# Kernel tuning notes

Hardware: AMD Instinct MI355X
Metric: run time of the kernel (lower is better)

Reference implementation:

```python
import jax, jax.numpy as jnp
import numpy as np

N_NODES = 50000
N_EDGES = 1_600_000
D_IN = 512
D_OUT = 512


def setup_inputs() -> dict:
    key = jax.random.key(0)
    k_x, k_w, k_b, k_r, k_c, k_e = jax.random.split(key, 6)
    x = jax.random.normal(k_x, (N_NODES, D_IN), dtype=jnp.float32)
    stdv = 1.0 / np.sqrt(D_OUT)
    weight = jax.random.uniform(k_w, (D_IN, D_OUT), minval=-stdv, maxval=stdv, dtype=jnp.float32)
    bias = jax.random.uniform(k_b, (D_OUT,), minval=-stdv, maxval=stdv, dtype=jnp.float32)
    row = jax.random.randint(k_r, (N_EDGES,), 0, N_NODES, dtype=jnp.int32)
    col = jax.random.randint(k_c, (N_EDGES,), 0, N_NODES, dtype=jnp.int32)
    edge_weight = jax.random.uniform(k_e, (N_EDGES,), dtype=jnp.float32)
    return {"x": x, "weight": weight, "bias": bias, "row": row, "col": col, "edge_weight": edge_weight}


def reference(x, weight, bias, row, col, edge_weight):
    # support = X @ W   [N, D_OUT]
    support = x @ weight
    # spmm: out[i] = sum_{e: row[e]==i} edge_weight[e] * support[col[e]]
    msgs = edge_weight[:, None] * support[col]  # [E, D_OUT]
    out = jax.ops.segment_sum(msgs, row, num_segments=N_NODES)
    return out + bias
```

## Files before the change

### kernel.cpp

```cpp
#include <hip/hip_runtime.h>
#include <hip/hip_fp16.h>

#define D_DIM 512
#define BM 128
#define BN 128
#define BK 64

typedef _Float16 h8 __attribute__((ext_vector_type(8)));
typedef _Float16 h4 __attribute__((ext_vector_type(4)));
typedef float f32x4 __attribute__((ext_vector_type(4)));

#define LDS_PTR(p) ((__attribute__((address_space(3))) void*)(p))
#define GLB_PTR(p) ((const __attribute__((address_space(1))) void*)(p))


__global__ void k_zero(int* __restrict__ counts, int n) {
    int i = blockIdx.x * blockDim.x + threadIdx.x;
    if (i < n) counts[i] = 0;
}

__global__ void k_count(const int* __restrict__ row, int* __restrict__ counts, int E) {
    int e = blockIdx.x * blockDim.x + threadIdx.x;
    if (e < E) atomicAdd(&counts[row[e]], 1);
}

__global__ void k_scan_part(const int* __restrict__ counts, int* __restrict__ offsets,
                            int* __restrict__ bsum, int n) {
    __shared__ int s[1024];
    int t = threadIdx.x;
    int i = blockIdx.x * 1024 + t;
    int v = (i < n) ? counts[i] : 0;
    s[t] = v;
    __syncthreads();
    for (int off = 1; off < 1024; off <<= 1) {
        int x = (t >= off) ? s[t - off] : 0;
        __syncthreads();
        s[t] += x;
        __syncthreads();
    }
    if (i < n) offsets[i] = s[t] - v;
    if (t == 1023) bsum[blockIdx.x] = s[t];
}

__global__ void k_scan_top(int* __restrict__ bsum, int* __restrict__ offsets, int nb, int n) {
    int t = threadIdx.x;
    int v = (t < nb) ? bsum[t] : 0;
    int orig = v;
    for (int off = 1; off < 64; off <<= 1) {
        int u = __shfl_up(v, off, 64);
        if (t >= off) v += u;
    }
    if (t < nb) bsum[t] = v - orig;
    if (t == nb - 1) offsets[n] = v;
}

__global__ void k_scan_add(int* __restrict__ offsets, int* __restrict__ cursor,
                           const int* __restrict__ bsum, int n) {
    int i = blockIdx.x * 1024 + threadIdx.x;
    if (i < n) {
        int o = offsets[i] + bsum[blockIdx.x];
        offsets[i] = o;
        cursor[i] = o;
    }
}

__global__ void k_scatter(const int* __restrict__ row, const int* __restrict__ col,
                          const float* __restrict__ ew, int* __restrict__ cursor,
                          uint2* __restrict__ packed, int E) {
    int e = blockIdx.x * blockDim.x + threadIdx.x;
    if (e < E) {
        int r = row[e];
        int pos = atomicAdd(&cursor[r], 1);
        packed[pos] = make_uint2((unsigned)col[e], __float_as_uint(ew[e]));
    }
}


__global__ void k_wt(const float* __restrict__ w, _Float16* __restrict__ wt) {
    __shared__ _Float16 tile[32][33];
    int bx = blockIdx.x & 15, by = blockIdx.x >> 4;
    int tx = threadIdx.x & 31, ty = threadIdx.x >> 5;
    for (int r = 0; r < 32; r += 8)
        tile[ty + r][tx] = (_Float16)w[(size_t)(by * 32 + ty + r) * 512 + bx * 32 + tx];
    __syncthreads();
    for (int r = 0; r < 32; r += 8)
        wt[(size_t)(bx * 32 + ty + r) * 512 + by * 32 + tx] = tile[tx][ty + r];
}


__launch_bounds__(256)
__global__ void k_gemm(const float* __restrict__ x, const _Float16* __restrict__ wt,
                       _Float16* __restrict__ sup, int M) {
    __shared__ __align__(16) unsigned char As[BM * BK * 2];
    __shared__ __align__(16) unsigned char Bs[BN * BK * 2];

    const int t = threadIdx.x;
    const int lane = t & 63, w = t >> 6;
    const int wr = w >> 1, wc = w & 1;
    const int m0 = blockIdx.x * BM, n0 = blockIdx.y * BN;

    f32x4 acc[4][4] = {};

    const int ar_t = t >> 4;
    const int ac_t = (t & 15) * 4;
    const int bn_t = t >> 3;
    const int bk_sw = ((t & 7) * 16) ^ (((t >> 3) & 7) << 4);

    for (int kt = 0; kt < D_DIM / BK; ++kt) {
        const int k0 = kt * BK;
        for (int j = 0; j < 4; ++j) {
            int n = j * 32 + bn_t;
            const char* src = (const char*)(wt + (size_t)(n0 + n) * 512 + k0) + bk_sw;
            __builtin_amdgcn_global_load_lds(GLB_PTR(src), LDS_PTR(Bs + j * 4096 + t * 16),
                                             16, 0, 0);
        }
        for (int i = 0; i < 8; ++i) {
            int r = i * 16 + ar_t;
            int g = m0 + r;
            if (g >= M) g = M - 1;
            const float4 v = *(const float4*)(x + (size_t)g * 512 + k0 + ac_t);
            h4 hv;
            hv[0] = (_Float16)v.x; hv[1] = (_Float16)v.y;
            hv[2] = (_Float16)v.z; hv[3] = (_Float16)v.w;
            int addr = r * 128 + ((ac_t * 2) ^ ((r & 7) << 4));
            *(h4*)(As + addr) = hv;
        }
        __syncthreads();

        for (int ks = 0; ks < 2; ++ks) {
            h8 af[4], bf[4];
            const int kb = ks * 64 + ((lane >> 4) * 8) * 2;
#pragma unroll
            for (int mb = 0; mb < 4; ++mb) {
                int r = wr * 64 + mb * 16 + (lane & 15);
                af[mb] = *(const h8*)(As + r * 128 + (kb ^ ((r & 7) << 4)));
            }
#pragma unroll
            for (int nb = 0; nb < 4; ++nb) {
                int n = wc * 64 + nb * 16 + (lane & 15);
                bf[nb] = *(const h8*)(Bs + n * 128 + (kb ^ ((n & 7) << 4)));
            }
#pragma unroll
            for (int mb = 0; mb < 4; ++mb)
#pragma unroll
                for (int nb = 0; nb < 4; ++nb)
                    acc[mb][nb] = __builtin_amdgcn_mfma_f32_16x16x32_f16(
                        af[mb], bf[nb], acc[mb][nb], 0, 0, 0);
        }
        __syncthreads();
    }

    const int cr = (lane >> 4) * 4, cc = lane & 15;
#pragma unroll
    for (int mb = 0; mb < 4; ++mb) {
#pragma unroll
        for (int nb = 0; nb < 4; ++nb) {
            int gn = n0 + wc * 64 + nb * 16 + cc;
#pragma unroll
            for (int q = 0; q < 4; ++q) {
                int gm = m0 + wr * 64 + mb * 16 + cr + q;
                if (gm < M)
                    sup[(size_t)gm * 512 + gn] = (_Float16)acc[mb][nb][q];
            }
        }
    }
}


__global__ void k_spmm(const _Float16* __restrict__ sup, const uint2* __restrict__ packed,
                       const int* __restrict__ offsets, const float* __restrict__ bias,
                       float* __restrict__ out, int M) {
    const int i = blockIdx.x * 4 + (threadIdx.x >> 6);
    if (i >= M) return;
    const int l = threadIdx.x & 63;
    const int s0 = offsets[i], s1 = offsets[i + 1];
    const _Float16* __restrict__ supl = sup + l * 8;

    float acc[8];
    {
        const float4 b0 = *(const float4*)(bias + l * 8);
        const float4 b1 = *(const float4*)(bias + l * 8 + 4);
        acc[0] = b0.x; acc[1] = b0.y; acc[2] = b0.z; acc[3] = b0.w;
        acc[4] = b1.x; acc[5] = b1.y; acc[6] = b1.z; acc[7] = b1.w;
    }

    int e = s0;
    if ((e & 1) && e < s1) {
        uint2 p = packed[e];
        float wgt = __uint_as_float(p.y);
        h8 h = *(const h8*)(supl + (size_t)p.x * 512);
#pragma unroll
        for (int j = 0; j < 8; ++j) acc[j] += wgt * (float)h[j];
        ++e;
    }
    for (; e + 8 <= s1; e += 8) {
        const uint4 q0 = *(const uint4*)(packed + e);
        const uint4 q1 = *(const uint4*)(packed + e + 2);
        const uint4 q2 = *(const uint4*)(packed + e + 4);
        const uint4 q3 = *(const uint4*)(packed + e + 6);
        const h8 h0 = *(const h8*)(supl + (size_t)q0.x * 512);
        const h8 h1 = *(const h8*)(supl + (size_t)q0.z * 512);
        const h8 h2 = *(const h8*)(supl + (size_t)q1.x * 512);
        const h8 h3 = *(const h8*)(supl + (size_t)q1.z * 512);
        const h8 h4v = *(const h8*)(supl + (size_t)q2.x * 512);
        const h8 h5 = *(const h8*)(supl + (size_t)q2.z * 512);
        const h8 h6 = *(const h8*)(supl + (size_t)q3.x * 512);
        const h8 h7 = *(const h8*)(supl + (size_t)q3.z * 512);
        const float w0 = __uint_as_float(q0.y), w1 = __uint_as_float(q0.w);
        const float w2 = __uint_as_float(q1.y), w3 = __uint_as_float(q1.w);
        const float w4 = __uint_as_float(q2.y), w5 = __uint_as_float(q2.w);
        const float w6 = __uint_as_float(q3.y), w7 = __uint_as_float(q3.w);
#pragma unroll
        for (int j = 0; j < 8; ++j) {
            float a = acc[j];
            a += w0 * (float)h0[j];
            a += w1 * (float)h1[j];
            a += w2 * (float)h2[j];
            a += w3 * (float)h3[j];
            a += w4 * (float)h4v[j];
            a += w5 * (float)h5[j];
            a += w6 * (float)h6[j];
            a += w7 * (float)h7[j];
            acc[j] = a;
        }
    }
    for (; e < s1; ++e) {
        uint2 p = packed[e];
        float wgt = __uint_as_float(p.y);
        h8 h = *(const h8*)(supl + (size_t)p.x * 512);
#pragma unroll
        for (int j = 0; j < 8; ++j) acc[j] += wgt * (float)h[j];
    }

    float4 o0 = {acc[0], acc[1], acc[2], acc[3]};
    float4 o1 = {acc[4], acc[5], acc[6], acc[7]};
    *(float4*)(out + (size_t)i * 512 + l * 8) = o0;
    *(float4*)(out + (size_t)i * 512 + l * 8 + 4) = o1;
}


extern "C" void kernel_launch(void* const* d_in, const int* in_sizes, int n_in,
                              void* d_out, int out_size, void* d_ws, size_t ws_size,
                              hipStream_t stream) {
    const float* x      = (const float*)d_in[0];
    const float* weight = (const float*)d_in[1];
    const float* bias   = (const float*)d_in[2];
    const int*   row    = (const int*)d_in[3];
    const int*   col    = (const int*)d_in[4];
    const float* ew     = (const float*)d_in[5];
    const int M = in_sizes[0] / D_DIM;
    const int E = in_sizes[3];
    float* out = (float*)d_out;

    char* ws = (char*)d_ws;
    size_t off = 0;
    auto alloc = [&](size_t bytes) {
        void* p = ws + off;
        off = (off + bytes + 255) & ~(size_t)255;
        return p;
    };
    _Float16* sup  = (_Float16*)alloc((size_t)M * D_DIM * 2);
    _Float16* wt   = (_Float16*)alloc((size_t)512 * 512 * 2);
    int* counts    = (int*)alloc((size_t)M * 4);
    int* offsets   = (int*)alloc((size_t)(M + 1) * 4);
    int* cursor    = (int*)alloc((size_t)M * 4);
    int* bsum      = (int*)alloc(64 * 4);
    uint2* packed  = (uint2*)alloc((size_t)E * 8);
    (void)ws_size; (void)n_in; (void)out_size;

    k_zero<<<(M + 255) / 256, 256, 0, stream>>>(counts, M);
    k_count<<<(E + 255) / 256, 256, 0, stream>>>(row, counts, E);
    const int SB = (M + 1023) / 1024;
    k_scan_part<<<SB, 1024, 0, stream>>>(counts, offsets, bsum, M);
    k_scan_top<<<1, 64, 0, stream>>>(bsum, offsets, SB, M);
    k_scan_add<<<SB, 1024, 0, stream>>>(offsets, cursor, bsum, M);
    k_scatter<<<(E + 255) / 256, 256, 0, stream>>>(row, col, ew, cursor, packed, E);

    k_wt<<<256, 256, 0, stream>>>(weight, wt);
    dim3 gg((M + BM - 1) / BM, D_DIM / BN);
    k_gemm<<<gg, 256, 0, stream>>>(x, wt, sup, M);

    k_spmm<<<(M + 3) / 4, 256, 0, stream>>>(sup, packed, offsets, bias, out, M);
}
```

Measured before the change: 649.1 us.

## Widen GEMM tile to 128x256, remap blocks per XCD, use nontemporal SpMM I/O

The GEMM tile grows from 128x128 to 128x256, so each block covers half the output width. Each wave now computes 128x64 with 32 accumulators, which halves how often the x tile is re-read and converted. Block IDs are remapped so that neighbouring M tiles land on the same XCD, improving L2 locality. The SpMM uses nontemporal loads for the packed edge stream and nontemporal stores for the output, and the zero kernel becomes hipMemsetAsync. The larger tile raises register and LDS pressure and halves the number of GEMM blocks.

```diff
diff --git a/kernel.cpp b/kernel.cpp
--- a/kernel.cpp
+++ b/kernel.cpp
@@ -3,21 +3,17 @@
 
 #define D_DIM 512
 #define BM 128
-#define BN 128
+#define BN 256
 #define BK 64
 
 typedef _Float16 h8 __attribute__((ext_vector_type(8)));
 typedef _Float16 h4 __attribute__((ext_vector_type(4)));
 typedef float f32x4 __attribute__((ext_vector_type(4)));
+typedef unsigned int u32x4 __attribute__((ext_vector_type(4)));
 
 #define LDS_PTR(p) ((__attribute__((address_space(3))) void*)(p))
 #define GLB_PTR(p) ((const __attribute__((address_space(1))) void*)(p))
 
-
-__global__ void k_zero(int* __restrict__ counts, int n) {
-    int i = blockIdx.x * blockDim.x + threadIdx.x;
-    if (i < n) counts[i] = 0;
-}
 
 __global__ void k_count(const int* __restrict__ row, int* __restrict__ counts, int E) {
     int e = blockIdx.x * blockDim.x + threadIdx.x;
@@ -90,16 +86,20 @@
 
 __launch_bounds__(256)
 __global__ void k_gemm(const float* __restrict__ x, const _Float16* __restrict__ wt,
-                       _Float16* __restrict__ sup, int M) {
+                       _Float16* __restrict__ sup, int M, int nwg) {
     __shared__ __align__(16) unsigned char As[BM * BK * 2];
     __shared__ __align__(16) unsigned char Bs[BN * BK * 2];
 
+    const int orig = blockIdx.x;
+    const int q = nwg >> 3, r = nwg & 7;
+    const int xcd = orig & 7, idx = orig >> 3;
+    const int wgid = (xcd < r ? xcd * (q + 1) : r * (q + 1) + (xcd - r) * q) + idx;
+    const int m0 = (wgid >> 1) * BM, n0 = (wgid & 1) * BN;
+
     const int t = threadIdx.x;
     const int lane = t & 63, w = t >> 6;
-    const int wr = w >> 1, wc = w & 1;
-    const int m0 = blockIdx.x * BM, n0 = blockIdx.y * BN;
-
-    f32x4 acc[4][4] = {};
+
+    f32x4 acc[8][4] = {};
 
     const int ar_t = t >> 4;
     const int ac_t = (t & 15) * 4;
@@ -108,40 +108,40 @@
 
     for (int kt = 0; kt < D_DIM / BK; ++kt) {
         const int k0 = kt * BK;
-        for (int j = 0; j < 4; ++j) {
+        for (int j = 0; j < 8; ++j) {
             int n = j * 32 + bn_t;
             const char* src = (const char*)(wt + (size_t)(n0 + n) * 512 + k0) + bk_sw;
             __builtin_amdgcn_global_load_lds(GLB_PTR(src), LDS_PTR(Bs + j * 4096 + t * 16),
                                              16, 0, 0);
         }
         for (int i = 0; i < 8; ++i) {
-            int r = i * 16 + ar_t;
-            int g = m0 + r;
+            int rr = i * 16 + ar_t;
+            int g = m0 + rr;
             if (g >= M) g = M - 1;
             const float4 v = *(const float4*)(x + (size_t)g * 512 + k0 + ac_t);
             h4 hv;
             hv[0] = (_Float16)v.x; hv[1] = (_Float16)v.y;
             hv[2] = (_Float16)v.z; hv[3] = (_Float16)v.w;
-            int addr = r * 128 + ((ac_t * 2) ^ ((r & 7) << 4));
+            int addr = rr * 128 + ((ac_t * 2) ^ ((rr & 7) << 4));
             *(h4*)(As + addr) = hv;
         }
         __syncthreads();
 
         for (int ks = 0; ks < 2; ++ks) {
-            h8 af[4], bf[4];
-            const int kb = ks * 64 + ((lane >> 4) * 8) * 2;
-#pragma unroll
-            for (int mb = 0; mb < 4; ++mb) {
-                int r = wr * 64 + mb * 16 + (lane & 15);
-                af[mb] = *(const h8*)(As + r * 128 + (kb ^ ((r & 7) << 4)));
+            h8 af[8], bf[4];
+            const int kb = ks * 64 + ((lane >> 4) * 16);
+#pragma unroll
+            for (int mb = 0; mb < 8; ++mb) {
+                int rr = mb * 16 + (lane & 15);
+                af[mb] = *(const h8*)(As + rr * 128 + (kb ^ ((rr & 7) << 4)));
             }
 #pragma unroll
             for (int nb = 0; nb < 4; ++nb) {
-                int n = wc * 64 + nb * 16 + (lane & 15);
+                int n = w * 64 + nb * 16 + (lane & 15);
                 bf[nb] = *(const h8*)(Bs + n * 128 + (kb ^ ((n & 7) << 4)));
             }
 #pragma unroll
-            for (int mb = 0; mb < 4; ++mb)
+            for (int mb = 0; mb < 8; ++mb)
 #pragma unroll
                 for (int nb = 0; nb < 4; ++nb)
                     acc[mb][nb] = __builtin_amdgcn_mfma_f32_16x16x32_f16(
@@ -152,15 +152,15 @@
 
     const int cr = (lane >> 4) * 4, cc = lane & 15;
 #pragma unroll
-    for (int mb = 0; mb < 4; ++mb) {
+    for (int mb = 0; mb < 8; ++mb) {
 #pragma unroll
         for (int nb = 0; nb < 4; ++nb) {
-            int gn = n0 + wc * 64 + nb * 16 + cc;
-#pragma unroll
-            for (int q = 0; q < 4; ++q) {
-                int gm = m0 + wr * 64 + mb * 16 + cr + q;
+            int gn = n0 + w * 64 + nb * 16 + cc;
+#pragma unroll
+            for (int qq = 0; qq < 4; ++qq) {
+                int gm = m0 + mb * 16 + cr + qq;
                 if (gm < M)
-                    sup[(size_t)gm * 512 + gn] = (_Float16)acc[mb][nb][q];
+                    sup[(size_t)gm * 512 + gn] = (_Float16)acc[mb][nb][qq];
             }
         }
     }
@@ -194,22 +194,22 @@
         ++e;
     }
     for (; e + 8 <= s1; e += 8) {
-        const uint4 q0 = *(const uint4*)(packed + e);
-        const uint4 q1 = *(const uint4*)(packed + e + 2);
-        const uint4 q2 = *(const uint4*)(packed + e + 4);
-        const uint4 q3 = *(const uint4*)(packed + e + 6);
-        const h8 h0 = *(const h8*)(supl + (size_t)q0.x * 512);
-        const h8 h1 = *(const h8*)(supl + (size_t)q0.z * 512);
-        const h8 h2 = *(const h8*)(supl + (size_t)q1.x * 512);
-        const h8 h3 = *(const h8*)(supl + (size_t)q1.z * 512);
-        const h8 h4v = *(const h8*)(supl + (size_t)q2.x * 512);
-        const h8 h5 = *(const h8*)(supl + (size_t)q2.z * 512);
-        const h8 h6 = *(const h8*)(supl + (size_t)q3.x * 512);
-        const h8 h7 = *(const h8*)(supl + (size_t)q3.z * 512);
-        const float w0 = __uint_as_float(q0.y), w1 = __uint_as_float(q0.w);
-        const float w2 = __uint_as_float(q1.y), w3 = __uint_as_float(q1.w);
-        const float w4 = __uint_as_float(q2.y), w5 = __uint_as_float(q2.w);
-        const float w6 = __uint_as_float(q3.y), w7 = __uint_as_float(q3.w);
+        const u32x4 q0 = __builtin_nontemporal_load((const u32x4*)(packed + e));
+        const u32x4 q1 = __builtin_nontemporal_load((const u32x4*)(packed + e + 2));
+        const u32x4 q2 = __builtin_nontemporal_load((const u32x4*)(packed + e + 4));
+        const u32x4 q3 = __builtin_nontemporal_load((const u32x4*)(packed + e + 6));
+        const h8 h0 = *(const h8*)(supl + (size_t)q0[0] * 512);
+        const h8 h1 = *(const h8*)(supl + (size_t)q0[2] * 512);
+        const h8 h2 = *(const h8*)(supl + (size_t)q1[0] * 512);
+        const h8 h3 = *(const h8*)(supl + (size_t)q1[2] * 512);
+        const h8 h4v = *(const h8*)(supl + (size_t)q2[0] * 512);
+        const h8 h5 = *(const h8*)(supl + (size_t)q2[2] * 512);
+        const h8 h6 = *(const h8*)(supl + (size_t)q3[0] * 512);
+        const h8 h7 = *(const h8*)(supl + (size_t)q3[2] * 512);
+        const float w0 = __uint_as_float(q0[1]), w1 = __uint_as_float(q0[3]);
+        const float w2 = __uint_as_float(q1[1]), w3 = __uint_as_float(q1[3]);
+        const float w4 = __uint_as_float(q2[1]), w5 = __uint_as_float(q2[3]);
+        const float w6 = __uint_as_float(q3[1]), w7 = __uint_as_float(q3[3]);
 #pragma unroll
         for (int j = 0; j < 8; ++j) {
             float a = acc[j];
@@ -232,10 +232,10 @@
         for (int j = 0; j < 8; ++j) acc[j] += wgt * (float)h[j];
     }
 
-    float4 o0 = {acc[0], acc[1], acc[2], acc[3]};
-    float4 o1 = {acc[4], acc[5], acc[6], acc[7]};
-    *(float4*)(out + (size_t)i * 512 + l * 8) = o0;
-    *(float4*)(out + (size_t)i * 512 + l * 8 + 4) = o1;
+    f32x4 o0 = {acc[0], acc[1], acc[2], acc[3]};
+    f32x4 o1 = {acc[4], acc[5], acc[6], acc[7]};
+    __builtin_nontemporal_store(o0, (f32x4*)(out + (size_t)i * 512 + l * 8));
+    __builtin_nontemporal_store(o1, (f32x4*)(out + (size_t)i * 512 + l * 8 + 4));
 }
 
 
@@ -268,7 +268,7 @@
     uint2* packed  = (uint2*)alloc((size_t)E * 8);
     (void)ws_size; (void)n_in; (void)out_size;
 
-    k_zero<<<(M + 255) / 256, 256, 0, stream>>>(counts, M);
+    (void)hipMemsetAsync(counts, 0, (size_t)M * 4, stream);
     k_count<<<(E + 255) / 256, 256, 0, stream>>>(row, counts, E);
     const int SB = (M + 1023) / 1024;
     k_scan_part<<<SB, 1024, 0, stream>>>(counts, offsets, bsum, M);
@@ -277,8 +277,8 @@
     k_scatter<<<(E + 255) / 256, 256, 0, stream>>>(row, col, ew, cursor, packed, E);
 
     k_wt<<<256, 256, 0, stream>>>(weight, wt);
-    dim3 gg((M + BM - 1) / BM, D_DIM / BN);
-    k_gemm<<<gg, 256, 0, stream>>>(x, wt, sup, M);
+    const int nwg = ((M + BM - 1) / BM) * (D_DIM / BN);
+    k_gemm<<<nwg, 256, 0, stream>>>(x, wt, sup, M, nwg);
 
     k_spmm<<<(M + 3) / 4, 256, 0, stream>>>(sup, packed, offsets, bias, out, M);
 }
```

New measurement: 655.6 us. No clear change (+1.0%).
